# Kernel optimization log

Hardware: AMD Instinct MI355X
Metric: run time of the kernel (lower is better)

## Reference

```python
import jax, jax.numpy as jnp
import numpy as np

B, S, D, H = 4, 1024, 1024, 16
DK = D // H


def setup_inputs() -> dict:
    key = jax.random.key(0)
    ks = jax.random.split(key, 14)
    scale = 1.0 / np.sqrt(D)
    inp = {
        "Qx": jax.random.normal(ks[0], (B, S, D), jnp.float32),
        "Kx": jax.random.normal(ks[1], (B, S, D), jnp.float32),
        "Vx": jax.random.normal(ks[2], (B, S, D), jnp.float32),
        "prob_phn": jax.random.uniform(ks[3], (B, S, S), jnp.float32),
        "mask": jax.random.randint(ks[4], (B, S, S), 0, 2, jnp.int32),
        "lambda_val": 1,
        "Wq": jax.random.normal(ks[5], (D, D), jnp.float32) * scale,
        "bq": jnp.zeros((D,), jnp.float32),
        "Wk": jax.random.normal(ks[6], (D, D), jnp.float32) * scale,
        "bk": jnp.zeros((D,), jnp.float32),
        "Wv": jax.random.normal(ks[7], (D, D), jnp.float32) * scale,
        "bv": jnp.zeros((D,), jnp.float32),
        "Wo": jax.random.normal(ks[8], (D, D), jnp.float32) * scale,
        "bo": jnp.zeros((D,), jnp.float32),
    }
    return inp


def _split_heads(x):
    # [B,S,D] -> [B,H,S,DK]
    b, s, _ = x.shape
    return x.reshape(b, s, H, DK).transpose(0, 2, 1, 3)


def reference(Qx, Kx, Vx, prob_phn, mask, lambda_val, Wq, bq, Wk, bk, Wv, bv, Wo, bo):
    q = _split_heads(Qx @ Wq.T + bq)
    k = _split_heads(Kx @ Wk.T + bk)
    v = _split_heads(Vx @ Wv.T + bv)
    scores = jnp.einsum("bhqd,bhkd->bhqk", q, k) / jnp.sqrt(jnp.float32(DK))
    if lambda_val > 0:
        # prob_phn: [B,S,S] -> transpose last two dims, broadcast over heads
        scores = scores - lambda_val * jnp.swapaxes(prob_phn, -2, -1)[:, None]
    scores = jnp.where(mask[:, None] == 0, jnp.float32(-1e9), scores)
    probs = jax.nn.softmax(scores, axis=-1)
    attn = jnp.einsum("bhqk,bhkd->bhqd", probs, v)
    out = attn.transpose(0, 2, 1, 3).reshape(Qx.shape[0], Qx.shape[1], D)
    out = out @ Wo.T + bo
    return (out, mask)
```

## Files before the change

### kernel.cpp

```cpp
#include <hip/hip_runtime.h>
#include <hip/hip_bf16.h>
#include <cstdint>
#include <cstddef>

#define BB 4
#define SS 1024
#define DD 1024
#define HH 16
#define DKK 64

typedef unsigned short u16;
typedef __bf16 bf16_t;
typedef __attribute__((ext_vector_type(8))) bf16_t bf16x8;
typedef __attribute__((ext_vector_type(4))) float floatx4;

#define LOG2E 1.4426950408889634f
#define QKSCALE 0.18033688011112042f

static __device__ inline u16 f2bf(float f) {
    union { float f; unsigned u; } v; v.f = f;
    unsigned r = v.u + 0x7fffu + ((v.u >> 16) & 1u);
    return (u16)(r >> 16);
}

static __device__ inline void load16_lds(const void* g, void* l) {
    __builtin_amdgcn_global_load_lds(
        (const __attribute__((address_space(1))) unsigned int*)g,
        (__attribute__((address_space(3))) unsigned int*)l,
        16, 0, 0);
}

static __device__ inline int swz64(int row, int c) { return row * 64 + ((c ^ (row & 7)) * 8); }

static __device__ inline float lam_val(const int* p) {
    int v = *p;
    if (v >= -100000 && v <= 100000) return (float)v;
    union { int i; float f; } u; u.i = v; return u.f;
}

__global__ void prep_kernel(const float* __restrict__ Qx, const float* __restrict__ Kx,
                            const float* __restrict__ Vx,
                            const float* __restrict__ Wq, const float* __restrict__ Wk,
                            const float* __restrict__ Wv, const float* __restrict__ Wo,
                            const float* __restrict__ prob, const int* __restrict__ mask,
                            const int* __restrict__ lam_p,
                            u16* __restrict__ Xq, u16* __restrict__ Xk, u16* __restrict__ Xv,
                            u16* __restrict__ wq, u16* __restrict__ wk,
                            u16* __restrict__ wv, u16* __restrict__ wo,
                            u16* __restrict__ biasT, float* __restrict__ maskOut)
{
    __shared__ float tile[64][65];
    __shared__ u16 btile[64][68];
    const int blk = blockIdx.x, tid = threadIdx.x;

    if (blk >= 1024) {
        const int cb = blk - 1024;
        const int base = cb * 1024;
        const float* src; u16* dst; int off0;
        if (base < 3145728) {
            int s = base >> 20;  off0 = base & 1048575;
            src = (s == 0) ? Qx : (s == 1) ? Kx : Vx;
            dst = (s == 0) ? Xq : (s == 1) ? Xk : Xv;
        } else {
            int v2 = base - 3145728;
            int s = v2 >> 18;  off0 = v2 & 262143;
            src = (s == 0) ? Wq : (s == 1) ? Wk : (s == 2) ? Wv : Wo;
            dst = (s == 0) ? wq : (s == 1) ? wk : (s == 2) ? wv : wo;
        }
        const float4* s4 = (const float4*)src;
        #pragma unroll
        for (int r = 0; r < 2; ++r) {
            int i4 = off0 + r * 512 + tid * 2;
            float4 a  = s4[i4];
            float4 b2 = s4[i4 + 1];
            uint4 pk;
            pk.x = (unsigned)f2bf(a.x)  | ((unsigned)f2bf(a.y)  << 16);
            pk.y = (unsigned)f2bf(a.z)  | ((unsigned)f2bf(a.w)  << 16);
            pk.z = (unsigned)f2bf(b2.x) | ((unsigned)f2bf(b2.y) << 16);
            pk.w = (unsigned)f2bf(b2.z) | ((unsigned)f2bf(b2.w) << 16);
            *(uint4*)((ushort4*)dst + i4) = pk;
        }
        return;
    }

    const int b = blk >> 8;
    const int q0 = ((blk >> 4) & 15) * 64, k0 = (blk & 15) * 64;
    const int kt = blk & 15;
    #pragma unroll
    for (int rr = 0; rr < 4; ++rr) {
        int unit = rr * 256 + tid;
        int kl = unit >> 4, qi = unit & 15;
        float4 p4 = *(const float4*)&prob[((size_t)(b * SS + k0 + kl)) * SS + q0 + qi * 4];
        tile[kl][qi * 4 + 0] = p4.x;
        tile[kl][qi * 4 + 1] = p4.y;
        tile[kl][qi * 4 + 2] = p4.z;
        tile[kl][qi * 4 + 3] = p4.w;
    }
    __syncthreads();
    const float lamc = lam_val(lam_p) * LOG2E;
    #pragma unroll
    for (int rr = 0; rr < 4; ++rr) {
        int pair = rr * 256 + tid;
        int q = pair >> 4, k4 = pair & 15;
        size_t midx = ((size_t)(b * SS + q0 + q)) * SS + k0 + k4 * 4;
        int4 m4 = *(const int4*)&mask[midx];
        float p0 = tile[k4 * 4 + 0][q];
        float p1 = tile[k4 * 4 + 1][q];
        float p2 = tile[k4 * 4 + 2][q];
        float p3 = tile[k4 * 4 + 3][q];
        ushort4 bb;
        bb.x = f2bf((m4.x == 0) ? -1.5e9f : -lamc * p0);
        bb.y = f2bf((m4.y == 0) ? -1.5e9f : -lamc * p1);
        bb.z = f2bf((m4.z == 0) ? -1.5e9f : -lamc * p2);
        bb.w = f2bf((m4.w == 0) ? -1.5e9f : -lamc * p3);
        *(ushort4*)&btile[q][k4 * 4] = bb;
        if (maskOut) {
            float4 mf = { (float)m4.x, (float)m4.y, (float)m4.z, (float)m4.w };
            *(float4*)&maskOut[midx] = mf;
        }
    }
    __syncthreads();
    u16* bT = biasT + (size_t)(b * 16 + kt) * 65536;
    #pragma unroll
    for (int rr = 0; rr < 4; ++rr) {
        int idx = rr * 256 + tid;
        int j = idx >> 8, quad = (idx >> 6) & 3, ql = idx & 63;
        ushort4 v = *(const ushort4*)&btile[ql][j * 16 + quad * 4];
        *(ushort4*)&bT[(size_t)((j * 4 + quad) * 1024 + q0 + ql) * 4] = v;
    }
}

template <int MODE>
static __device__ inline void gemm_body(const u16* __restrict__ A, const u16* __restrict__ W,
                                        const float* __restrict__ bias,
                                        u16* __restrict__ Cb, float* __restrict__ Cf,
                                        int mBase, int nBase)
{
    constexpr int K = 1024, N = 1024;
    __shared__ __align__(16) u16 As[128 * 64];
    __shared__ __align__(16) u16 Bs[128 * 64];
    const int tid = threadIdx.x;
    const int wv = tid >> 6, ln = tid & 63, l15 = ln & 15, quad = ln >> 4;
    const int wm = (wv & 1) * 64, wn = (wv >> 1) * 64;

    const u16* Aptr[4]; const u16* Wptr[4];
    #pragma unroll
    for (int r = 0; r < 4; ++r) {
        int p = r * 256 + wv * 64 + ln;
        int row = p >> 3;
        int c = (p & 7) ^ (row & 7);
        Aptr[r] = A + (size_t)(mBase + row) * K + c * 8;
        Wptr[r] = W + (size_t)(nBase + row) * K + c * 8;
    }

    floatx4 acc[4][4] = {};

    for (int k0 = 0; k0 < K; k0 += 64) {
        __syncthreads();
        #pragma unroll
        for (int r = 0; r < 4; ++r) {
            load16_lds(Aptr[r] + k0, &As[(r * 256 + wv * 64) * 8]);
            load16_lds(Wptr[r] + k0, &Bs[(r * 256 + wv * 64) * 8]);
        }
        __syncthreads();
        #pragma unroll
        for (int t = 0; t < 2; ++t) {
            bf16x8 af[4], bfr[4];
            #pragma unroll
            for (int i = 0; i < 4; ++i)
                af[i] = *(const bf16x8*)&As[swz64(wm + i * 16 + l15, t * 4 + quad)];
            #pragma unroll
            for (int j = 0; j < 4; ++j)
                bfr[j] = *(const bf16x8*)&Bs[swz64(wn + j * 16 + l15, t * 4 + quad)];
            #pragma unroll
            for (int i = 0; i < 4; ++i)
                #pragma unroll
                for (int j = 0; j < 4; ++j)
                    acc[i][j] = __builtin_amdgcn_mfma_f32_16x16x32_bf16(af[i], bfr[j], acc[i][j], 0, 0, 0);
        }
    }

    #pragma unroll
    for (int i = 0; i < 4; ++i) {
        #pragma unroll
        for (int j = 0; j < 4; ++j) {
            int col = nBase + wn + j * 16 + l15;
            float bcol = bias[col];
            if (MODE == 2) {
                int hh = col >> 6, dk = col & 63;
                int row0 = mBase + wm + i * 16 + quad * 4;
                int bb = row0 >> 10, s = row0 & 1023;
                ushort4 v4;
                v4.x = f2bf(acc[i][j][0] + bcol);
                v4.y = f2bf(acc[i][j][1] + bcol);
                v4.z = f2bf(acc[i][j][2] + bcol);
                v4.w = f2bf(acc[i][j][3] + bcol);
                *(ushort4*)&Cb[((size_t)((bb * HH + hh) * DKK) + dk) * SS + s] = v4;
            } else {
                #pragma unroll
                for (int r = 0; r < 4; ++r) {
                    int row = mBase + wm + i * 16 + quad * 4 + r;
                    float v = acc[i][j][r] + bcol;
                    if (MODE == 1) Cf[(size_t)row * N + col] = v;
                    else           Cb[(size_t)row * N + col] = f2bf(v);
                }
            }
        }
    }
}

__global__ __launch_bounds__(256) void gemm_qkv_kernel(
    const u16* __restrict__ Xq, const u16* __restrict__ Xk, const u16* __restrict__ Xv,
    const u16* __restrict__ Wq, const u16* __restrict__ Wk, const u16* __restrict__ Wv,
    const float* __restrict__ bq, const float* __restrict__ bk, const float* __restrict__ bv,
    u16* __restrict__ Cq, u16* __restrict__ Ck, u16* __restrict__ Vtout)
{
    const int lin = blockIdx.x + 8 * blockIdx.y + 256 * blockIdx.z;
    const int sw  = (lin & 7) * 96 + (lin >> 3);
    const int x = sw & 7, y = (sw >> 3) & 31, z = sw >> 8;
    const int mBase = y * 128, nBase = x * 128;

    if (z == 2) {
        gemm_body<2>(Xv, Wv, bv, Vtout, nullptr, mBase, nBase);
    } else {
        const u16* A = (z == 0) ? Xq : Xk;
        const u16* W = (z == 0) ? Wq : Wk;
        const float* bias = (z == 0) ? bq : bk;
        u16* C = (z == 0) ? Cq : Ck;
        gemm_body<0>(A, W, bias, C, nullptr, mBase, nBase);
    }
}

__global__ __launch_bounds__(256) void gemm_out_kernel(
    const u16* __restrict__ A, const u16* __restrict__ W,
    const float* __restrict__ bias, float* __restrict__ Cf)
{
    const int lin = blockIdx.x + 8 * blockIdx.y;
    const int sw  = (lin & 7) * 32 + (lin >> 3);
    const int x = sw & 7, y = sw >> 3;
    gemm_body<1>(A, W, bias, nullptr, Cf, y * 128, x * 128);
}

__global__ __launch_bounds__(256) void attn_kernel(
    const u16* __restrict__ Qf, const u16* __restrict__ Kf,
    const u16* __restrict__ Vt, const u16* __restrict__ biasT,
    u16* __restrict__ Attn)
{
    __shared__ __align__(16) u16 Qs[64 * 64];
    __shared__ __align__(16) u16 Ks[64 * 64];
    __shared__ __align__(16) u16 Vs[64 * 64];
    __shared__ __align__(16) u16 Ps[4][16 * 72];
    const int tid = threadIdx.x;
    const int wv = tid >> 6, ln = tid & 63, l15 = ln & 15, quad = ln >> 4;

    const int lin = blockIdx.x + 16 * blockIdx.y + 256 * blockIdx.z;
    const int sw  = (lin & 7) * 128 + (lin >> 3);
    const int qt = sw & 15, h = (sw >> 4) & 15, b = sw >> 8;
    const int q0 = qt * 64;

    int row64[2], col64[2];
    #pragma unroll
    for (int r = 0; r < 2; ++r) {
        int p = r * 256 + wv * 64 + ln;
        row64[r] = p >> 3;
        col64[r] = ((p & 7) ^ (row64[r] & 7)) * 8;
    }

    #pragma unroll
    for (int r = 0; r < 2; ++r)
        load16_lds(Qf + ((size_t)(b * SS + q0 + row64[r])) * DD + h * DKK + col64[r],
                   &Qs[(r * 256 + wv * 64) * 8]);
    __syncthreads();

    bf16x8 aq[2];
    #pragma unroll
    for (int t = 0; t < 2; ++t)
        aq[t] = *(const bf16x8*)&Qs[swz64(wv * 16 + l15, t * 4 + quad)];

    const size_t vt_head = ((size_t)(b * HH + h)) * DKK * SS;
    const u16* Kp[2]; const u16* Vp[2];
    #pragma unroll
    for (int r = 0; r < 2; ++r) {
        Kp[r] = Kf + ((size_t)(b * SS + row64[r])) * DD + h * DKK + col64[r];
        Vp[r] = Vt + vt_head + (size_t)row64[r] * SS + col64[r];
    }

    const int qq = q0 + wv * 16 + l15;
    const u16* bpT = biasT + (size_t)b * 1048576 + (size_t)quad * 4096 + (size_t)qq * 4;

    floatx4 o[4] = {};
    float rsum = 0.f;

    for (int kt = 0; kt < 16; ++kt) {
        const int kk0 = kt * 64;
        __syncthreads();
        #pragma unroll
        for (int r = 0; r < 2; ++r) {
            load16_lds(Kp[r] + (size_t)kk0 * DD, &Ks[(r * 256 + wv * 64) * 8]);
            load16_lds(Vp[r] + kk0, &Vs[(r * 256 + wv * 64) * 8]);
        }
        __syncthreads();

        uint2 braw[4];
        #pragma unroll
        for (int j = 0; j < 4; ++j)
            braw[j] = *(const uint2*)&bpT[(size_t)kt * 65536 + j * 16384];

        floatx4 sfr[4];
        #pragma unroll
        for (int j = 0; j < 4; ++j) {
            bf16x8 bk0 = *(const bf16x8*)&Ks[swz64(j * 16 + l15, quad)];
            bf16x8 bk1 = *(const bf16x8*)&Ks[swz64(j * 16 + l15, 4 + quad)];
            floatx4 s = {};
            s = __builtin_amdgcn_mfma_f32_16x16x32_bf16(bk0, aq[0], s, 0, 0, 0);
            sfr[j] = __builtin_amdgcn_mfma_f32_16x16x32_bf16(bk1, aq[1], s, 0, 0, 0);
        }

        #pragma unroll
        for (int j = 0; j < 4; ++j) {
            float b0 = __uint_as_float(braw[j].x << 16);
            float b1 = __uint_as_float(braw[j].x & 0xffff0000u);
            float b2 = __uint_as_float(braw[j].y << 16);
            float b3 = __uint_as_float(braw[j].y & 0xffff0000u);
            float p0 = __builtin_amdgcn_exp2f(fmaf(sfr[j][0], QKSCALE, b0));
            float p1 = __builtin_amdgcn_exp2f(fmaf(sfr[j][1], QKSCALE, b1));
            float p2 = __builtin_amdgcn_exp2f(fmaf(sfr[j][2], QKSCALE, b2));
            float p3 = __builtin_amdgcn_exp2f(fmaf(sfr[j][3], QKSCALE, b3));
            rsum += (p0 + p1) + (p2 + p3);
            uint2 pk;
            pk.x = (__float_as_uint(p0) >> 16) | (__float_as_uint(p1) & 0xffff0000u);
            pk.y = (__float_as_uint(p2) >> 16) | (__float_as_uint(p3) & 0xffff0000u);
            *(uint2*)&Ps[wv][l15 * 72 + j * 16 + quad * 4] = pk;
        }

        #pragma unroll
        for (int t = 0; t < 2; ++t) {
            bf16x8 ap = *(const bf16x8*)&Ps[wv][l15 * 72 + t * 32 + quad * 8];
            #pragma unroll
            for (int j = 0; j < 4; ++j) {
                bf16x8 bvv = *(const bf16x8*)&Vs[swz64(j * 16 + l15, t * 4 + quad)];
                o[j] = __builtin_amdgcn_mfma_f32_16x16x32_bf16(bvv, ap, o[j], 0, 0, 0);
            }
        }
    }

    rsum += __shfl_xor(rsum, 16);
    rsum += __shfl_xor(rsum, 32);
    const float ri = 1.0f / rsum;

    u16* outp = Attn + ((size_t)(b * SS + qq)) * DD + h * DKK + quad * 4;
    #pragma unroll
    for (int j = 0; j < 4; ++j) {
        ushort4 v4;
        v4.x = f2bf(o[j][0] * ri);
        v4.y = f2bf(o[j][1] * ri);
        v4.z = f2bf(o[j][2] * ri);
        v4.w = f2bf(o[j][3] * ri);
        *(ushort4*)&outp[j * 16] = v4;
    }
}

extern "C" void kernel_launch(void* const* d_in, const int* in_sizes, int n_in,
                              void* d_out, int out_size, void* d_ws, size_t ws_size,
                              hipStream_t stream)
{
    const float* Qx  = (const float*)d_in[0];
    const float* Kx  = (const float*)d_in[1];
    const float* Vx  = (const float*)d_in[2];
    const float* prob = (const float*)d_in[3];
    const int*   mask = (const int*)d_in[4];
    const int*   lam  = (const int*)d_in[5];
    const float* Wq  = (const float*)d_in[6];
    const float* bq  = (const float*)d_in[7];
    const float* Wk  = (const float*)d_in[8];
    const float* bk  = (const float*)d_in[9];
    const float* Wv  = (const float*)d_in[10];
    const float* bv  = (const float*)d_in[11];
    const float* Wo  = (const float*)d_in[12];
    const float* bo  = (const float*)d_in[13];

    char* ws = (char*)d_ws;
    const size_t MB = 1024 * 1024;
    u16*   Xq     = (u16*)(ws + 0 * MB);
    u16*   Xk     = (u16*)(ws + 8 * MB);
    u16*   Xv     = (u16*)(ws + 16 * MB);
    u16*   wq     = (u16*)(ws + 24 * MB);
    u16*   wk     = (u16*)(ws + 26 * MB);
    u16*   wvp    = (u16*)(ws + 28 * MB);
    u16*   wo     = (u16*)(ws + 30 * MB);
    u16*   q_flat = (u16*)(ws + 32 * MB);
    u16*   k_flat = (u16*)(ws + 40 * MB);
    u16*   vt     = (u16*)(ws + 56 * MB);
    u16*   biasT  = (u16*)(ws + 64 * MB);
    u16*   attn   = (u16*)(ws + 80 * MB);

    float* maskOut = (out_size >= 2 * BB * SS * DD) ? (float*)d_out + (size_t)BB * SS * DD
                                                    : nullptr;

    prep_kernel<<<5120, 256, 0, stream>>>(Qx, Kx, Vx, Wq, Wk, Wv, Wo, prob, mask, lam,
                                          Xq, Xk, Xv, wq, wk, wvp, wo, biasT, maskOut);
    gemm_qkv_kernel<<<dim3(8, 32, 3), 256, 0, stream>>>(Xq, Xk, Xv, wq, wk, wvp,
                                                        bq, bk, bv, q_flat, k_flat, vt);
    attn_kernel<<<dim3(16, 16, 4), 256, 0, stream>>>(q_flat, k_flat, vt, biasT, attn);
    gemm_out_kernel<<<dim3(8, 32, 1), 256, 0, stream>>>(attn, wo, bo, (float*)d_out);
}
```

Measured before the change: 252.7 us.

## Double-buffer LDS tiles in projection GEMMs to overlap loads with MFMA

Converts the QKV and output projection GEMM main loops from single-buffered LDS staging to a ping-pong double buffer. The next K-tile's global-to-LDS loads are issued before computing on the current tile, and one barrier per tile replaces two. This is meant to hide global load latency behind MFMA work. LDS use per block doubles to 64KB, which may cut occupancy.

New measurement: 250.7 us. No clear change (-0.8%).

```diff
diff --git a/kernel.cpp b/kernel.cpp
--- a/kernel.cpp
+++ b/kernel.cpp
@@ -134,11 +134,10 @@
 static __device__ inline void gemm_body(const u16* __restrict__ A, const u16* __restrict__ W,
                                         const float* __restrict__ bias,
                                         u16* __restrict__ Cb, float* __restrict__ Cf,
-                                        int mBase, int nBase)
+                                        int mBase, int nBase,
+                                        u16* As0, u16* Bs0, u16* As1, u16* Bs1)
 {
     constexpr int K = 1024, N = 1024;
-    __shared__ __align__(16) u16 As[128 * 64];
-    __shared__ __align__(16) u16 Bs[128 * 64];
     const int tid = threadIdx.x;
     const int wv = tid >> 6, ln = tid & 63, l15 = ln & 15, quad = ln >> 4;
     const int wm = (wv & 1) * 64, wn = (wv >> 1) * 64;
@@ -155,30 +154,47 @@
 
     floatx4 acc[4][4] = {};
 
-    for (int k0 = 0; k0 < K; k0 += 64) {
+#define G_STAGE(k0, Ad, Bd)                                              \
+    {                                                                    \
+        _Pragma("unroll")                                                \
+        for (int r = 0; r < 4; ++r) {                                    \
+            load16_lds(Aptr[r] + (k0), &Ad[(r * 256 + wv * 64) * 8]);    \
+            load16_lds(Wptr[r] + (k0), &Bd[(r * 256 + wv * 64) * 8]);    \
+        }                                                                \
+    }
+
+#define G_COMPUTE(Asrc, Bsrc)                                            \
+    {                                                                    \
+        _Pragma("unroll")                                                \
+        for (int t = 0; t < 2; ++t) {                                    \
+            bf16x8 af[4], bfr[4];                                        \
+            _Pragma("unroll")                                            \
+            for (int i = 0; i < 4; ++i)                                  \
+                af[i] = *(const bf16x8*)&Asrc[swz64(wm + i * 16 + l15, t * 4 + quad)]; \
+            _Pragma("unroll")                                            \
+            for (int j = 0; j < 4; ++j)                                  \
+                bfr[j] = *(const bf16x8*)&Bsrc[swz64(wn + j * 16 + l15, t * 4 + quad)]; \
+            _Pragma("unroll")                                            \
+            for (int i = 0; i < 4; ++i)                                  \
+                _Pragma("unroll")                                        \
+                for (int j = 0; j < 4; ++j)                              \
+                    acc[i][j] = __builtin_amdgcn_mfma_f32_16x16x32_bf16(af[i], bfr[j], acc[i][j], 0, 0, 0); \
+        }                                                                \
+    }
+
+    G_STAGE(0, As0, Bs0);
+    __syncthreads();
+
+    for (int k0 = 0; k0 < K; k0 += 128) {
+        if (k0 + 64 < K) G_STAGE(k0 + 64, As1, Bs1);
+        G_COMPUTE(As0, Bs0);
         __syncthreads();
-        #pragma unroll
-        for (int r = 0; r < 4; ++r) {
-            load16_lds(Aptr[r] + k0, &As[(r * 256 + wv * 64) * 8]);
-            load16_lds(Wptr[r] + k0, &Bs[(r * 256 + wv * 64) * 8]);
-        }
+        if (k0 + 128 < K) G_STAGE(k0 + 128, As0, Bs0);
+        G_COMPUTE(As1, Bs1);
         __syncthreads();
-        #pragma unroll
-        for (int t = 0; t < 2; ++t) {
-            bf16x8 af[4], bfr[4];
-            #pragma unroll
-            for (int i = 0; i < 4; ++i)
-                af[i] = *(const bf16x8*)&As[swz64(wm + i * 16 + l15, t * 4 + quad)];
-            #pragma unroll
-            for (int j = 0; j < 4; ++j)
-                bfr[j] = *(const bf16x8*)&Bs[swz64(wn + j * 16 + l15, t * 4 + quad)];
-            #pragma unroll
-            for (int i = 0; i < 4; ++i)
-                #pragma unroll
-                for (int j = 0; j < 4; ++j)
-                    acc[i][j] = __builtin_amdgcn_mfma_f32_16x16x32_bf16(af[i], bfr[j], acc[i][j], 0, 0, 0);
-        }
-    }
+    }
+#undef G_STAGE
+#undef G_COMPUTE
 
     #pragma unroll
     for (int i = 0; i < 4; ++i) {
@@ -215,19 +231,24 @@
     const float* __restrict__ bq, const float* __restrict__ bk, const float* __restrict__ bv,
     u16* __restrict__ Cq, u16* __restrict__ Ck, u16* __restrict__ Vtout)
 {
+    __shared__ __align__(16) u16 As0[128 * 64];
+    __shared__ __align__(16) u16 Bs0[128 * 64];
+    __shared__ __align__(16) u16 As1[128 * 64];
+    __shared__ __align__(16) u16 Bs1[128 * 64];
+
     const int lin = blockIdx.x + 8 * blockIdx.y + 256 * blockIdx.z;
     const int sw  = (lin & 7) * 96 + (lin >> 3);
     const int x = sw & 7, y = (sw >> 3) & 31, z = sw >> 8;
     const int mBase = y * 128, nBase = x * 128;
 
     if (z == 2) {
-        gemm_body<2>(Xv, Wv, bv, Vtout, nullptr, mBase, nBase);
+        gemm_body<2>(Xv, Wv, bv, Vtout, nullptr, mBase, nBase, As0, Bs0, As1, Bs1);
     } else {
         const u16* A = (z == 0) ? Xq : Xk;
         const u16* W = (z == 0) ? Wq : Wk;
         const float* bias = (z == 0) ? bq : bk;
         u16* C = (z == 0) ? Cq : Ck;
-        gemm_body<0>(A, W, bias, C, nullptr, mBase, nBase);
+        gemm_body<0>(A, W, bias, C, nullptr, mBase, nBase, As0, Bs0, As1, Bs1);
     }
 }
 
@@ -235,10 +256,15 @@
     const u16* __restrict__ A, const u16* __restrict__ W,
     const float* __restrict__ bias, float* __restrict__ Cf)
 {
+    __shared__ __align__(16) u16 As0[128 * 64];
+    __shared__ __align__(16) u16 Bs0[128 * 64];
+    __shared__ __align__(16) u16 As1[128 * 64];
+    __shared__ __align__(16) u16 Bs1[128 * 64];
+
     const int lin = blockIdx.x + 8 * blockIdx.y;
     const int sw  = (lin & 7) * 32 + (lin >> 3);
     const int x = sw & 7, y = sw >> 3;
-    gemm_body<1>(A, W, bias, nullptr, Cf, y * 128, x * 128);
+    gemm_body<1>(A, W, bias, nullptr, Cf, y * 128, x * 128, As0, Bs0, As1, Bs1);
 }
 
 __global__ __launch_bounds__(256) void attn_kernel(
```
